# Optimization experiments

Hardware: AMD Instinct MI355X
Metric: run time of the kernel (lower is better)

The kernel has to match this reference:

```python
import jax, jax.numpy as jnp
import numpy as np

B, L, W, S, STEPS, VOCAB, NLAB = 1024, 128, 512, 8, 12, 32, 10

def setup_inputs() -> dict:
    key = jax.random.key(0)
    ks = jax.random.split(key, 24)
    def nrm(k, shape, scale=0.05):
        return jax.random.normal(k, shape, jnp.float32) * scale
    x = jax.random.randint(ks[0], (B, L), 0, VOCAB)
    embed = nrm(ks[1], (VOCAB, W), 0.1).at[0].set(0.0)  # padding_idx=0
    return {
        'x': x,
        'embed': embed,
        'W_mix': nrm(ks[2], (W, 3 * W)), 'b_mix': jnp.zeros((W,), jnp.float32),
        'W_in': nrm(ks[3], (S, W, 2 * W)), 'b_in': jnp.zeros((S, W), jnp.float32),
        'W_link': nrm(ks[4], (S, W, W)), 'b_link': jnp.zeros((S, W), jnp.float32),
        'W_ih': nrm(ks[5], (S, 3 * W, W)), 'b_ih': jnp.zeros((S, 3 * W), jnp.float32),
        'W_hh': nrm(ks[6], (S, 3 * W, W)), 'b_hh': jnp.zeros((S, 3 * W), jnp.float32),
        'W_gate': nrm(ks[7], (S, 1, W)), 'b_gate': jnp.zeros((S, 1), jnp.float32),
        'phase': nrm(ks[8], (S, W), 0.5), 'prism_gain': jnp.zeros((S, W), jnp.float32),
        'W_delta': nrm(ks[9], (S, W, W)), 'b_delta': jnp.zeros((S, W), jnp.float32),
        'decay_param': jnp.zeros((), jnp.float32),
        'W_out': nrm(ks[10], (NLAB, W)), 'b_out': jnp.zeros((NLAB,), jnp.float32),
    }

def _encode(x, embed, W_mix, b_mix):
    emb = embed[x]                                          # [B,L,W]
    mask = (x != 0).astype(jnp.float32)[..., None]          # [B,L,1]
    summed = (emb * mask).sum(1)
    denom = jnp.maximum(mask.sum(1), 1.0)
    mean = summed / denom
    maxed = jnp.where(mask == 0, -10000.0, emb).max(1)
    maxed = jnp.where(jnp.isfinite(maxed), maxed, 0.0)
    last_idx = jnp.maximum(mask[..., 0].sum(1).astype(jnp.int32) - 1, 0)
    last = jnp.take_along_axis(emb, last_idx[:, None, None], axis=1)[:, 0]
    cat = jnp.concatenate([mean, maxed, last], -1)          # [B,3W]
    return jnp.tanh(cat @ W_mix.T + b_mix)

def _forward(x, embed, W_mix, b_mix, W_in, b_in, W_link, b_link, W_ih, b_ih,
             W_hh, b_hh, W_gate, b_gate, phase, prism_gain, W_delta, b_delta,
             decay_param, W_out, b_out):
    summary = _encode(x, embed, W_mix, b_mix)               # [B,W]
    decay = jax.nn.sigmoid(decay_param)
    inv_sqrt_s = np.float32(1.0 / np.sqrt(S))
    gain = jax.nn.softplus(prism_gain)[None]                # [1,S,W]

    def step(carry, _):
        h, hs = carry
        shared = jnp.concatenate([h, summary], -1)          # conditioned: [B,2W]
        f0 = jnp.tanh(jnp.einsum('swi,bi->bsw', W_in, shared) + b_in)      # [B,S,W]
        prev = jnp.roll(f0, 1, axis=1)                      # sparse ring: feats[(i-1)%S]
        feats = jnp.tanh(f0 + jnp.einsum('sow,bsw->bso', W_link, prev) + b_link)
        # recurrent side pockets: per-side GRUCell (torch gate order r,z,n)
        gi = jnp.einsum('sgw,bsw->bsg', W_ih, feats) + b_ih
        gh = jnp.einsum('sgw,bsw->bsg', W_hh, hs) + b_hh
        ir, iz, inn = jnp.split(gi, 3, -1)
        hr, hz, hn = jnp.split(gh, 3, -1)
        r = jax.nn.sigmoid(ir + hr)
        z = jax.nn.sigmoid(iz + hz)
        n = jnp.tanh(inn + r * hn)
        hs_new = (1.0 - z) * n + z * hs                     # [B,S,W]
        feat = hs_new
        gate = jax.nn.sigmoid(jnp.einsum('sow,bsw->bso', W_gate, feat) + b_gate)  # [B,S,1]
        feat = jnp.cos(feat + phase[None]) ** 2 * gain      # prismion
        upd = gate * jnp.tanh(jnp.einsum('sow,bsw->bso', W_delta, feat) + b_delta)
        delta = upd.sum(1) * inv_sqrt_s
        h_new = jnp.tanh(h * decay + delta)
        return (h_new, hs_new), None

    hs0 = jnp.zeros((B, S, W), jnp.float32)
    (h, _), _ = jax.lax.scan(step, (summary, hs0), None, length=STEPS)
    return h @ W_out.T + b_out                               # [B,10]

def reference(x, embed, W_mix, b_mix, W_in, b_in, W_link, b_link, W_ih, b_ih,
              W_hh, b_hh, W_gate, b_gate, phase, prism_gain, W_delta, b_delta,
              decay_param, W_out, b_out):
    return _forward(x, embed, W_mix, b_mix, W_in, b_in, W_link, b_link, W_ih,
                    b_ih, W_hh, b_hh, W_gate, b_gate, phase, prism_gain,
                    W_delta, b_delta, decay_param, W_out, b_out)
```

## Files before the change

### kernel.cpp

```cpp
#include <hip/hip_runtime.h>
#include <hip/hip_bf16.h>


typedef unsigned short u16;
typedef __attribute__((ext_vector_type(8))) short short8;
typedef __attribute__((ext_vector_type(4))) float f32x4;

__device__ __forceinline__ float bf2f(u16 v) {
    union { unsigned int u; float f; } x; x.u = ((unsigned int)v) << 16; return x.f;
}
__device__ __forceinline__ u16 f2bf(float f) {
    union { float f; unsigned int u; } x; x.f = f;
    unsigned int u = x.u;
    return (u16)((u + 0x7FFFu + ((u >> 16) & 1u)) >> 16);
}
__device__ __forceinline__ float fsig(float v) {
    return __builtin_amdgcn_rcpf(1.f + __expf(-v));
}
__device__ __forceinline__ float ftanh(float v) {
    return 1.f - 2.f * __builtin_amdgcn_rcpf(__expf(2.f * v) + 1.f);
}
__device__ __forceinline__ float fsoftplus(float v) {
    return (v > 20.f) ? v : __logf(1.f + __expf(v));
}

union U4 { ushort4 v; u16 e[4]; };

__device__ __forceinline__ void gload_lds16(const u16* g, u16* l) {
    __builtin_amdgcn_global_load_lds(
        (const __attribute__((address_space(1))) unsigned int*)g,
        (__attribute__((address_space(3))) unsigned int*)l, 16, 0, 0);
}

__device__ __forceinline__ int sane16(u16 u) {
    if ((u & 0x7FFF) == 0) return 1;
    int e = (u >> 7) & 0xFF;
    return (e >= 0x33 && e <= 0x43) ? 1 : 0;
}
__global__ __launch_bounds__(256) void detect_k(const u16* __restrict__ raw,
                                                int* __restrict__ flag) {
    const int t = threadIdx.x;
    int c = sane16(raw[1024 + t * 2]) + sane16(raw[1024 + t * 2 + 1]);
#pragma unroll
    for (int off = 32; off; off >>= 1) c += __shfl_down(c, off, 64);
    __shared__ int red[4];
    if ((t & 63) == 0) red[t >> 6] = c;
    __syncthreads();
    if (t == 0) *flag = (red[0] + red[1] + red[2] + red[3] >= 448) ? 1 : 0;
}

struct CT { const void* src[20]; int n[20]; int off[20]; };
__global__ __launch_bounds__(256) void conv_k(CT ct, u16* __restrict__ dstBase,
                                              const int* __restrict__ flag) {
    const int isbf = *flag;
    const int gid = blockIdx.x * 256 + threadIdx.x;
    const int stride = gridDim.x * 256;
    for (int tn = 0; tn < 20; ++tn) {
        const int n = ct.n[tn];
        const int n4 = n >> 2;
        u16* dst = dstBase + ct.off[tn];
        if (!isbf) {
            const float* s = (const float*)ct.src[tn];
            for (int i = gid; i < n4; i += stride) {
                f32x4 v = *(const f32x4*)(s + i * 4);
                *(ushort4*)(dst + i * 4) =
                    make_ushort4(f2bf(v[0]), f2bf(v[1]), f2bf(v[2]), f2bf(v[3]));
            }
            if (gid < (n & 3)) { int i = n4 * 4 + gid; dst[i] = f2bf(s[i]); }
        } else {
            const u16* s = (const u16*)ct.src[tn];
            for (int i = gid; i < n4; i += stride)
                *(ushort4*)(dst + i * 4) = *(const ushort4*)(s + i * 4);
            if (gid < (n & 3)) { int i = n4 * 4 + gid; dst[i] = s[i]; }
        }
    }
}

__global__ __launch_bounds__(256) void pack_k(const u16* __restrict__ Wih,
                                              const u16* __restrict__ Whh,
                                              u16* __restrict__ Wcat) {
    long i = ((long)blockIdx.x * 256 + threadIdx.x) * 8;
    if (i >= 8L * 1536 * 512) return;
    long sg = i >> 9;
    long k  = i & 511;
    *(short8*)(Wcat + sg * 1024 + k)       = *(const short8*)(Wih + i);
    *(short8*)(Wcat + sg * 1024 + 512 + k) = *(const short8*)(Whh + i);
}

struct GP {
    const u16* A;  long lda; long aOff[8];
    const u16* Bw; long ldb; long bwOff[8];
    const u16* bias; long biasOff[8];
    const u16* add; long ldadd; long addOff;
    const float* gate_pre;
    const u16* bgate;
    void* C; long ldc; long cOff[8];
    float* C2;
    u16* C3;
    int K; int nt;
};

template<int EPI, int MT, int SWZ, int PIPE, int NK>
__global__ __launch_bounds__(256) void gemm_k(GP p) {
    constexpr int MW   = MT / 32;
    constexpr int AITS = MT / 32;
    constexpr int NBUF = PIPE ? 3 : 2;
    __shared__ __align__(16) u16 lA[NBUF][MT * 64];
    __shared__ __align__(16) u16 lB[NBUF][128 * 64];
    const int t    = threadIdx.x;
    const int lane = t & 63;
    const int wv   = t >> 6;
    int bx = blockIdx.x, byy = blockIdx.y;
    if (SWZ) {
        int wgid = bx + (byy << 5);
        bx  = ((wgid & 7) << 2) + ((wgid >> 3) & 3);
        byy = wgid >> 5;
    }
    const int z    = bx / p.nt;
    const int n0   = (bx - z * p.nt) * 128;
    const int m0   = byy * MT;

    const u16* Ab = p.A + p.aOff[z] + (long)m0 * p.lda;
    const u16* Bb = p.Bw + p.bwOff[z] + (long)n0 * p.ldb;

    f32x4 acc[MW][4];
#pragma unroll
    for (int i = 0; i < MW; i++)
#pragma unroll
        for (int j = 0; j < 4; j++) acc[i][j] = (f32x4){0.f, 0.f, 0.f, 0.f};

    const int wm   = (wv & 1) * (MT / 2);
    const int wn   = (wv >> 1) * 64;
    const int fr   = lane & 15;
    const int quad = lane >> 4;

    auto stage = [&](int buf, long kb) {
#pragma unroll
        for (int it = 0; it < AITS; ++it) {
            int flat = it * 256 + t, row = flat >> 3, src = (flat & 7) ^ (row & 7);
            gload_lds16(Ab + (long)row * p.lda + kb + src * 8, &lA[buf][flat * 8]);
        }
#pragma unroll
        for (int it = 0; it < 4; ++it) {
            int flat = it * 256 + t, row = flat >> 3, src = (flat & 7) ^ (row & 7);
            gload_lds16(Bb + (long)row * p.ldb + kb + src * 8, &lB[buf][flat * 8]);
        }
    };
    auto inner = [&](int cur) {
#pragma unroll
        for (int kk = 0; kk < 2; ++kk) {
            const int q = kk * 4 + quad;
            short8 aF[MW], bF[4];
#pragma unroll
            for (int mi = 0; mi < MW; mi++) {
                int row = wm + mi * 16 + fr;
                aF[mi] = *(const short8*)&lA[cur][row * 64 + (q ^ (row & 7)) * 8];
            }
#pragma unroll
            for (int ni = 0; ni < 4; ni++) {
                int row = wn + ni * 16 + fr;
                bF[ni] = *(const short8*)&lB[cur][row * 64 + (q ^ (row & 7)) * 8];
            }
#pragma unroll
            for (int mi = 0; mi < MW; mi++)
#pragma unroll
                for (int ni = 0; ni < 4; ni++)
                    acc[mi][ni] = __builtin_amdgcn_mfma_f32_16x16x32_bf16(
                        aF[mi], bF[ni], acc[mi][ni], 0, 0, 0);
        }
    };

    if (PIPE == 0) {
        const int nk = p.K >> 6;
        stage(0, 0);
        __syncthreads();
        for (int kt = 0; kt < nk; ++kt) {
            const int cur = kt & 1, nxt = cur ^ 1;
            if (kt + 1 < nk) stage(nxt, (long)(kt + 1) * 64);
            inner(cur);
            __syncthreads();
        }
    } else {
        stage(0, 0); stage(1, 64);
        asm volatile("s_waitcnt vmcnt(6)" ::: "memory");
        __builtin_amdgcn_s_barrier();
#pragma unroll
        for (int kt = 0; kt < NK; ++kt) {
            if (kt + 2 < NK) stage((kt + 2) % 3, (long)(kt + 2) * 64);
            inner(kt % 3);
            if (kt + 1 < NK) {
                if (kt + 2 < NK)
                    asm volatile("s_waitcnt vmcnt(6) lgkmcnt(0)" ::: "memory");
                else
                    asm volatile("s_waitcnt vmcnt(0) lgkmcnt(0)" ::: "memory");
                __builtin_amdgcn_s_barrier();
            }
        }
    }

    float sgv[MW][4];
    if (EPI == 3) {
#pragma unroll
        for (int mi = 0; mi < MW; mi++)
#pragma unroll
            for (int r = 0; r < 4; r++) {
                long row = m0 + wm + mi * 16 + quad * 4 + r;
                sgv[mi][r] = fsig(p.gate_pre[row * 8 + z] + bf2f(p.bgate[z]));
            }
    }

#pragma unroll
    for (int mi = 0; mi < MW; mi++) {
#pragma unroll
        for (int ni = 0; ni < 4; ni++) {
            const int mg = m0 + wm + mi * 16 + quad * 4;
            const int ng = n0 + wn + ni * 16 + fr;
#pragma unroll
            for (int r = 0; r < 4; r++) {
                float v = acc[mi][ni][r];
                const long row = mg + r;
                if (EPI == 1) {
                    float ad = bf2f(p.add[z * p.addOff + row * p.ldadd + ng]);
                    v = ftanh(v + ad + bf2f(p.bias[p.biasOff[z] + ng]));
                    ((u16*)p.C)[p.cOff[z] + row * p.ldc + ng] = f2bf(v);
                } else if (EPI == 3) {
                    v = ftanh(v + bf2f(p.bias[p.biasOff[z] + ng])) * sgv[mi][r];
                    ((u16*)p.C)[p.cOff[z] + row * p.ldc + ng] = f2bf(v);
                } else if (EPI == 4) {
                    v = ftanh(v + bf2f(p.bias[ng]));
                    u16 b = f2bf(v);
                    ((u16*)p.C)[row * 512 + ng] = b;
                    p.C3[row * 512 + ng] = b;
                    p.C2[row * 512 + ng] = v;
                } else if (EPI == 6) {
                    v = v + bf2f(p.bias[p.biasOff[z] + ng]);
                    ((u16*)p.C)[p.cOff[z] + row * p.ldc + ng] = f2bf(v);
                } else {
                    float ad = bf2f(p.add[row * p.ldadd + ng]);
                    v = ftanh(v + ad);
                    ((u16*)p.C)[row * p.ldc + ng] = f2bf(v);
                }
            }
        }
    }
}

struct GGP {
    const u16* fhs_in;
    u16* fhs_out;
    const u16* Wcat;
    const u16* b_ih;
    const u16* b_hh;
    u16* prism;
    float* gate_pre;
    const u16* Wg;
    const u16* phase;
    const u16* pgain;
};

__global__ __launch_bounds__(512, 2) void grug_k(GGP p) {
    __shared__ __align__(16) u16 sA[2][128 * 32];
    __shared__ __align__(16) u16 sW[3][3][128 * 32];
    const int t    = threadIdx.x;
    const int lane = t & 63;
    const int wv   = t >> 6;
    const int wgid = blockIdx.x + (blockIdx.y << 5);
    const int s    = wgid & 7;
    const int idx  = wgid >> 3;
    const int w0   = (idx & 3) * 128;
    const int m0   = (idx >> 2) * 128;
    const int fr   = lane & 15;
    const int quad = lane >> 4;
    const int wm   = (wv & 1) * 64;
    const int wn   = (wv >> 1) * 32;

    const u16* Ab = p.fhs_in + (long)m0 * 8192 + (long)s * 1024;
    const u16* Wb = p.Wcat + (long)s * 1536 * 1024;

    f32x4 acc[4][4][2];
#pragma unroll
    for (int q = 0; q < 4; q++)
#pragma unroll
        for (int mi = 0; mi < 4; mi++)
#pragma unroll
            for (int ni = 0; ni < 2; ni++) acc[q][mi][ni] = (f32x4){0.f,0.f,0.f,0.f};

    const int arow = t >> 2, ac4 = t & 3, asrc = ac4 ^ ((arow >> 1) & 3);

    auto stageA = [&](int buf, int kt) {
        gload_lds16(Ab + (long)arow * 8192 + kt * 32 + asrc * 8, &sA[buf][t * 8]);
    };
    auto stageWq = [&](int buf, int kt, int q) {
        long g = (long)(q * 512 + w0 + arow);
        gload_lds16(Wb + g * 1024 + kt * 32 + asrc * 8, &sW[buf][q][t * 8]);
    };

    stageA(0, 0);
    stageWq(0, 0, 0); stageWq(0, 0, 1); stageWq(0, 0, 2);
    stageWq(1, 1, 0); stageWq(1, 1, 1); stageWq(1, 1, 2);
    asm volatile("s_waitcnt vmcnt(3)" ::: "memory");
    __builtin_amdgcn_s_barrier();

    int aCur = 0, wCur = 0;
    for (int kt = 0; kt < 32; ++kt) {
        const int aNxt = aCur ^ 1;
        int wNx2 = wCur + 2; if (wNx2 >= 3) wNx2 -= 3;
        short8 aF[4], bF0[2], bF1[2], bF2[2];

#pragma unroll
        for (int mi = 0; mi < 4; mi++) {
            int row = wm + mi * 16 + fr;
            aF[mi] = *(const short8*)&sA[aCur][row * 32 + ((quad ^ ((row >> 1) & 3)) & 3) * 8];
        }
#pragma unroll
        for (int ni = 0; ni < 2; ni++) {
            int row = wn + ni * 16 + fr;
            bF0[ni] = *(const short8*)&sW[wCur][0][row * 32 + ((quad ^ ((row >> 1) & 3)) & 3) * 8];
        }
        if (kt + 1 < 32) stageA(aNxt, kt + 1);
        if (kt + 2 < 32) stageWq(wNx2, kt + 2, 0);
        __builtin_amdgcn_s_barrier();
        asm volatile("s_waitcnt lgkmcnt(0)" ::: "memory");
        __builtin_amdgcn_s_setprio(1);
#pragma unroll
        for (int mi = 0; mi < 4; mi++)
#pragma unroll
            for (int ni = 0; ni < 2; ni++)
                acc[0][mi][ni] = __builtin_amdgcn_mfma_f32_16x16x32_bf16(aF[mi], bF0[ni], acc[0][mi][ni], 0, 0, 0);
        __builtin_amdgcn_s_setprio(0);
        __builtin_amdgcn_s_barrier();

#pragma unroll
        for (int ni = 0; ni < 2; ni++) {
            int row = wn + ni * 16 + fr;
            bF1[ni] = *(const short8*)&sW[wCur][1][row * 32 + ((quad ^ ((row >> 1) & 3)) & 3) * 8];
        }
        if (kt + 2 < 32) stageWq(wNx2, kt + 2, 1);
        __builtin_amdgcn_s_barrier();
        asm volatile("s_waitcnt lgkmcnt(0)" ::: "memory");
        __builtin_amdgcn_s_setprio(1);
#pragma unroll
        for (int mi = 0; mi < 4; mi++)
#pragma unroll
            for (int ni = 0; ni < 2; ni++)
                acc[1][mi][ni] = __builtin_amdgcn_mfma_f32_16x16x32_bf16(aF[mi], bF1[ni], acc[1][mi][ni], 0, 0, 0);
        __builtin_amdgcn_s_setprio(0);
        __builtin_amdgcn_s_barrier();

#pragma unroll
        for (int ni = 0; ni < 2; ni++) {
            int row = wn + ni * 16 + fr;
            bF2[ni] = *(const short8*)&sW[wCur][2][row * 32 + ((quad ^ ((row >> 1) & 3)) & 3) * 8];
        }
        if (kt + 2 < 32) stageWq(wNx2, kt + 2, 2);
        if (kt < 30)       asm volatile("s_waitcnt vmcnt(3) lgkmcnt(0)" ::: "memory");
        else if (kt == 30) asm volatile("s_waitcnt vmcnt(0) lgkmcnt(0)" ::: "memory");
        else               asm volatile("s_waitcnt lgkmcnt(0)" ::: "memory");
        __builtin_amdgcn_s_setprio(1);
        if (kt < 16) {
#pragma unroll
            for (int mi = 0; mi < 4; mi++)
#pragma unroll
                for (int ni = 0; ni < 2; ni++)
                    acc[2][mi][ni] = __builtin_amdgcn_mfma_f32_16x16x32_bf16(aF[mi], bF2[ni], acc[2][mi][ni], 0, 0, 0);
        } else {
#pragma unroll
            for (int mi = 0; mi < 4; mi++)
#pragma unroll
                for (int ni = 0; ni < 2; ni++)
                    acc[3][mi][ni] = __builtin_amdgcn_mfma_f32_16x16x32_bf16(aF[mi], bF2[ni], acc[3][mi][ni], 0, 0, 0);
        }
        __builtin_amdgcn_s_setprio(0);
        __builtin_amdgcn_s_barrier();

        aCur = aNxt;
        wCur += 1; if (wCur >= 3) wCur -= 3;
    }

    const u16* bih = p.b_ih + (long)s * 1536;
    const u16* bhh = p.b_hh + (long)s * 1536;
    float gp[4][4];
#pragma unroll
    for (int mi = 0; mi < 4; mi++)
#pragma unroll
        for (int r = 0; r < 4; r++) gp[mi][r] = 0.f;

#pragma unroll
    for (int ni = 0; ni < 2; ni++) {
        const int col = w0 + wn + ni * 16 + fr;
        const float br  = bf2f(bih[col])        + bf2f(bhh[col]);
        const float bz  = bf2f(bih[512 + col])  + bf2f(bhh[512 + col]);
        const float bin = bf2f(bih[1024 + col]);
        const float bhn = bf2f(bhh[1024 + col]);
        const float ph  = bf2f(p.phase[s * 512 + col]);
        const float gain = fsoftplus(bf2f(p.pgain[s * 512 + col]));
        const float wg  = bf2f(p.Wg[s * 512 + col]);
#pragma unroll
        for (int mi = 0; mi < 4; mi++) {
#pragma unroll
            for (int r = 0; r < 4; r++) {
                const long b = m0 + wm + mi * 16 + quad * 4 + r;
                float rv = fsig(acc[0][mi][ni][r] + br);
                float zv = fsig(acc[1][mi][ni][r] + bz);
                float nv = ftanh(acc[2][mi][ni][r] + bin + rv * (acc[3][mi][ni][r] + bhn));
                float hold = bf2f(p.fhs_in[b * 8192 + s * 1024 + 512 + col]);
                float hv = (1.f - zv) * nv + zv * hold;
                p.fhs_out[b * 8192 + s * 1024 + 512 + col] = f2bf(hv);
                float c = __cosf(hv + ph);
                p.prism[b * 4096 + s * 512 + col] = f2bf(c * c * gain);
                gp[mi][r] += wg * hv;
            }
        }
    }
#pragma unroll
    for (int m = 1; m < 16; m <<= 1)
#pragma unroll
        for (int mi = 0; mi < 4; mi++)
#pragma unroll
            for (int r = 0; r < 4; r++) gp[mi][r] += __shfl_xor(gp[mi][r], m, 64);
    if (fr == 0) {
#pragma unroll
        for (int mi = 0; mi < 4; mi++)
#pragma unroll
            for (int r = 0; r < 4; r++) {
                long b = m0 + wm + mi * 16 + quad * 4 + r;
                atomicAdd(&p.gate_pre[b * 8 + s], gp[mi][r]);
            }
    }
}

__global__ __launch_bounds__(256) void encode_k(const int* __restrict__ x,
                                                const u16* __restrict__ embed,
                                                u16* __restrict__ cat) {
    __shared__ int toks[128];
    __shared__ int cnt_s;
    const int b = blockIdx.x, t = threadIdx.x;
    if (t < 128) toks[t] = x[b * 128 + t];
    __syncthreads();
    if (t == 0) {
        int c = 0;
        for (int l = 0; l < 128; l++) c += (toks[l] != 0);
        cnt_s = c;
    }
    __syncthreads();
    const int cnt = cnt_s;
    const int lastTok = toks[cnt > 0 ? cnt - 1 : 0];
    for (int w = t; w < 512; w += 256) {
        float sum = 0.f, mx = -10000.f;
        for (int l = 0; l < 128; l++) {
            int tok = toks[l];
            if (tok != 0) {
                float e = bf2f(embed[tok * 512 + w]);
                sum += e;
                mx = fmaxf(mx, e);
            }
        }
        float mean = sum / (float)(cnt > 0 ? cnt : 1);
        float last = bf2f(embed[lastTok * 512 + w]);
        cat[(long)b * 1536 + w]        = f2bf(mean);
        cat[(long)b * 1536 + 512 + w]  = f2bf(mx);
        cat[(long)b * 1536 + 1024 + w] = f2bf(last);
    }
}

__global__ __launch_bounds__(256) void hupd_k(const u16* __restrict__ upd,
                                              float* __restrict__ h,
                                              u16* __restrict__ h_b,
                                              const u16* __restrict__ decay_p,
                                              float* __restrict__ gate_pre) {
    const int idx = blockIdx.x * 256 + threadIdx.x;
    if (idx < 8192) gate_pre[idx] = 0.f;
    const int b = idx >> 9, w = idx & 511;
    const long base = (long)b * 4096 + w;
    float dsum = 0.f;
#pragma unroll
    for (int s = 0; s < 8; s++) dsum += bf2f(upd[base + s * 512]);
    const float decay = fsig(bf2f(decay_p[0]));
    const float hv = ftanh(h[idx] * decay + dsum * 0.35355339059327373f);
    h[idx] = hv;
    h_b[idx] = f2bf(hv);
}

__global__ __launch_bounds__(64) void out_k(const float* __restrict__ h,
                                            const u16* __restrict__ Wout,
                                            const u16* __restrict__ bout,
                                            void* __restrict__ out,
                                            const int* __restrict__ flag) {
    const int b = blockIdx.x, lane = threadIdx.x;
    const int isbf = *flag;
    for (int j = 0; j < 10; j++) {
        float p = 0.f;
#pragma unroll
        for (int k = 0; k < 8; k++) {
            int w = lane + k * 64;
            p += h[(long)b * 512 + w] * bf2f(Wout[j * 512 + w]);
        }
#pragma unroll
        for (int off = 32; off; off >>= 1) p += __shfl_down(p, off, 64);
        if (lane == 0) {
            float val = p + bf2f(bout[j]);
            if (isbf) ((u16*)out)[b * 10 + j] = f2bf(val);
            else      ((float*)out)[b * 10 + j] = val;
        }
    }
}

extern "C" void kernel_launch(void* const* d_in, const int* in_sizes, int n_in,
                              void* d_out, int out_size, void* d_ws, size_t ws_size,
                              hipStream_t stream) {
    (void)n_in; (void)out_size; (void)ws_size;
    const int* x = (const int*)d_in[0];

    char* pp = (char*)d_ws;
    auto carve = [&](size_t n) { char* r = pp; pp += (n + 255) & ~(size_t)255; return (void*)r; };

    CT ct;
    size_t ctot = 0;
    for (int i = 0; i < 20; i++) {
        ct.src[i] = d_in[i + 1];
        ct.n[i]   = in_sizes[i + 1];
        ct.off[i] = (int)ctot;
        ctot += ((size_t)in_sizes[i + 1] + 15) & ~(size_t)15;
    }
    u16* canon = (u16*)carve(ctot * 2);
    const u16* embed  = canon + ct.off[0];
    const u16* W_mix  = canon + ct.off[1];
    const u16* b_mix  = canon + ct.off[2];
    const u16* W_in   = canon + ct.off[3];
    const u16* b_in   = canon + ct.off[4];
    const u16* W_link = canon + ct.off[5];
    const u16* b_link = canon + ct.off[6];
    const u16* W_ih   = canon + ct.off[7];
    const u16* b_ih   = canon + ct.off[8];
    const u16* W_hh   = canon + ct.off[9];
    const u16* b_hh   = canon + ct.off[10];
    const u16* W_gate = canon + ct.off[11];
    const u16* b_gate = canon + ct.off[12];
    const u16* phase  = canon + ct.off[13];
    const u16* pgain  = canon + ct.off[14];
    const u16* W_delta= canon + ct.off[15];
    const u16* b_delta= canon + ct.off[16];
    const u16* decayp = canon + ct.off[17];
    const u16* W_out  = canon + ct.off[18];
    const u16* b_out  = canon + ct.off[19];

    int*   flag   = (int*)  carve(256);
    u16*   Wcat   = (u16*)  carve((size_t)8 * 1536 * 1024 * 2);
    u16*   cat    = (u16*)  carve((size_t)1024 * 1536 * 2);
    u16*   h_b    = (u16*)  carve((size_t)1024 * 512 * 2);
    u16*   summ_b = (u16*)  carve((size_t)1024 * 512 * 2);
    float* h      = (float*)carve((size_t)1024 * 512 * 4);
    u16*   cin    = (u16*)  carve((size_t)1024 * 4096 * 2);
    u16*   f0     = (u16*)  carve((size_t)1024 * 4096 * 2);
    u16*   fhs0   = (u16*)  carve((size_t)1024 * 8192 * 2);
    u16*   fhs1   = (u16*)  carve((size_t)1024 * 8192 * 2);
    u16*   prism  = (u16*)  carve((size_t)1024 * 4096 * 2);
    u16*   upd    = (u16*)  carve((size_t)1024 * 4096 * 2);
    float* gate_pre = (float*)carve((size_t)1024 * 8 * 4);

    (void)hipMemsetAsync(fhs0, 0, (size_t)1024 * 8192 * 2, stream);
    (void)hipMemsetAsync(fhs1, 0, (size_t)1024 * 8192 * 2, stream);
    (void)hipMemsetAsync(gate_pre, 0, (size_t)1024 * 8 * 4, stream);

    detect_k<<<dim3(1), dim3(256), 0, stream>>>((const u16*)d_in[1], flag);
    conv_k<<<dim3(1024), dim3(256), 0, stream>>>(ct, canon, flag);
    pack_k<<<dim3(3072), dim3(256), 0, stream>>>(W_ih, W_hh, Wcat);
    encode_k<<<dim3(1024), dim3(256), 0, stream>>>(x, embed, cat);

    {
        GP p{}; p.A = cat; p.lda = 1536; p.Bw = W_mix; p.ldb = 1536;
        p.bias = b_mix; p.C = h_b; p.ldc = 512; p.C2 = h; p.C3 = summ_b;
        p.K = 1536; p.nt = 4;
        gemm_k<4, 64, 0, 0, 0><<<dim3(4, 16, 1), dim3(256), 0, stream>>>(p);
    }
    {
        GP p{}; p.A = summ_b; p.lda = 512; p.Bw = W_in + 512; p.ldb = 1024;
        p.bias = b_in; p.C = cin; p.ldc = 4096; p.K = 512; p.nt = 32;
        gemm_k<6, 64, 1, 1, 8><<<dim3(32, 16, 1), dim3(256), 0, stream>>>(p);
    }

    for (int step = 0; step < 12; ++step) {
        u16* fhs_cur = (step & 1) ? fhs1 : fhs0;
        u16* fhs_nxt = (step & 1) ? fhs0 : fhs1;
        {
            GP p{}; p.A = h_b; p.lda = 512; p.Bw = W_in; p.ldb = 1024;
            p.add = cin; p.ldadd = 4096; p.C = f0; p.ldc = 4096;
            p.K = 512; p.nt = 32;
            gemm_k<7, 64, 1, 1, 8><<<dim3(32, 16, 1), dim3(256), 0, stream>>>(p);
        }
        {
            GP p{}; p.A = f0; p.lda = 4096;
            for (int s = 0; s < 8; s++) p.aOff[s] = (long)((s + 7) & 7) * 512;
            p.Bw = W_link; p.ldb = 512;
            for (int s = 0; s < 8; s++) p.bwOff[s] = (long)s * 512 * 512;
            p.bias = b_link;
            for (int s = 0; s < 8; s++) p.biasOff[s] = (long)s * 512;
            p.add = f0; p.ldadd = 4096; p.addOff = 512;
            p.C = fhs_cur; p.ldc = 8192;
            for (int s = 0; s < 8; s++) p.cOff[s] = (long)s * 1024;
            p.K = 512; p.nt = 4;
            gemm_k<1, 64, 1, 1, 8><<<dim3(32, 16, 1), dim3(256), 0, stream>>>(p);
        }
        {
            GGP g{};
            g.fhs_in = fhs_cur; g.fhs_out = fhs_nxt; g.Wcat = Wcat;
            g.b_ih = b_ih; g.b_hh = b_hh; g.prism = prism; g.gate_pre = gate_pre;
            g.Wg = W_gate; g.phase = phase; g.pgain = pgain;
            grug_k<<<dim3(32, 8, 1), dim3(512), 0, stream>>>(g);
        }
        {
            GP p{}; p.A = prism; p.lda = 4096;
            for (int s = 0; s < 8; s++) p.aOff[s] = (long)s * 512;
            p.Bw = W_delta; p.ldb = 512;
            for (int s = 0; s < 8; s++) p.bwOff[s] = (long)s * 512 * 512;
            p.bias = b_delta;
            for (int s = 0; s < 8; s++) p.biasOff[s] = (long)s * 512;
            p.gate_pre = gate_pre; p.bgate = b_gate;
            p.C = upd; p.ldc = 4096;
            for (int s = 0; s < 8; s++) p.cOff[s] = (long)s * 512;
            p.K = 512; p.nt = 4;
            gemm_k<3, 64, 1, 1, 8><<<dim3(32, 16, 1), dim3(256), 0, stream>>>(p);
        }
        hupd_k<<<dim3(2048), dim3(256), 0, stream>>>(upd, h, h_b, decayp, gate_pre);
    }

    out_k<<<dim3(1024), dim3(64), 0, stream>>>(h, W_out, b_out, d_out, flag);
}
```

Measured before the change: 1.499 ms.

## Add 128x128 eight-wave GEMM with interleaved stage/MFMA pipeline for K=512 GEMMs

Adds a new gemm8_k kernel with 512 threads, 128x128 tiles, a 32-wide K step and triple-buffered LDS. It splits each K step into two MFMA halves, interleaved with A and B global-to-LDS prefetches and raised wave priority, to hide load latency. All per-step K=512 GEMMs switch to it, halving the grid to 256 blocks. The risk is lower occupancy and more barriers per K step, and the fixed 16-iteration loop hardcodes K=512.

```diff
diff --git a/kernel.cpp b/kernel.cpp
--- a/kernel.cpp
+++ b/kernel.cpp
@@ -100,13 +100,12 @@
     int K; int nt;
 };
 
-template<int EPI, int MT, int SWZ, int PIPE, int NK>
+template<int EPI, int MT, int SWZ>
 __global__ __launch_bounds__(256) void gemm_k(GP p) {
     constexpr int MW   = MT / 32;
     constexpr int AITS = MT / 32;
-    constexpr int NBUF = PIPE ? 3 : 2;
-    __shared__ __align__(16) u16 lA[NBUF][MT * 64];
-    __shared__ __align__(16) u16 lB[NBUF][128 * 64];
+    __shared__ __align__(16) u16 lA[2][MT * 64];
+    __shared__ __align__(16) u16 lB[2][128 * 64];
     const int t    = threadIdx.x;
     const int lane = t & 63;
     const int wv   = t >> 6;
@@ -170,38 +169,124 @@
         }
     };
 
-    if (PIPE == 0) {
-        const int nk = p.K >> 6;
-        stage(0, 0);
+    const int nk = p.K >> 6;
+    stage(0, 0);
+    __syncthreads();
+    for (int kt = 0; kt < nk; ++kt) {
+        const int cur = kt & 1, nxt = cur ^ 1;
+        if (kt + 1 < nk) stage(nxt, (long)(kt + 1) * 64);
+        inner(cur);
         __syncthreads();
-        for (int kt = 0; kt < nk; ++kt) {
-            const int cur = kt & 1, nxt = cur ^ 1;
-            if (kt + 1 < nk) stage(nxt, (long)(kt + 1) * 64);
-            inner(cur);
-            __syncthreads();
-        }
-    } else {
-        stage(0, 0); stage(1, 64);
-        asm volatile("s_waitcnt vmcnt(6)" ::: "memory");
+    }
+
+#pragma unroll
+    for (int mi = 0; mi < MW; mi++) {
+#pragma unroll
+        for (int ni = 0; ni < 4; ni++) {
+            const int mg = m0 + wm + mi * 16 + quad * 4;
+            const int ng = n0 + wn + ni * 16 + fr;
+#pragma unroll
+            for (int r = 0; r < 4; r++) {
+                float v = acc[mi][ni][r];
+                const long row = mg + r;
+                if (EPI == 4) {
+                    v = ftanh(v + bf2f(p.bias[ng]));
+                    u16 b = f2bf(v);
+                    ((u16*)p.C)[row * 512 + ng] = b;
+                    p.C3[row * 512 + ng] = b;
+                    p.C2[row * 512 + ng] = v;
+                }
+            }
+        }
+    }
+}
+
+template<int EPI>
+__global__ __launch_bounds__(512, 2) void gemm8_k(GP p) {
+    __shared__ __align__(16) u16 lA[3][128 * 32];
+    __shared__ __align__(16) u16 lB[3][128 * 32];
+    const int t    = threadIdx.x;
+    const int lane = t & 63;
+    const int wv   = t >> 6;
+    const int wgid = blockIdx.x + (blockIdx.y << 5);
+    const int zc   = wgid & 7;
+    const int ct   = zc * 4 + ((wgid >> 3) & 3);
+    const int m0   = (wgid >> 5) * 128;
+    const int z    = ct / p.nt;
+    const int n0   = (ct - z * p.nt) * 128;
+    const int fr   = lane & 15;
+    const int quad = lane >> 4;
+    const int wm   = (wv & 1) * 64;
+    const int wn   = (wv >> 1) * 32;
+
+    const u16* Ab = p.A + p.aOff[z] + (long)m0 * p.lda;
+    const u16* Bb = p.Bw + p.bwOff[z] + (long)n0 * p.ldb;
+
+    f32x4 acc[4][2];
+#pragma unroll
+    for (int mi = 0; mi < 4; mi++)
+#pragma unroll
+        for (int ni = 0; ni < 2; ni++) acc[mi][ni] = (f32x4){0.f, 0.f, 0.f, 0.f};
+
+    const int arow = t >> 2, ac4 = t & 3, asrc = ac4 ^ ((arow >> 1) & 3);
+
+    auto stageA = [&](int buf, int kt) {
+        gload_lds16(Ab + (long)arow * p.lda + kt * 32 + asrc * 8, &lA[buf][t * 8]);
+    };
+    auto stageB = [&](int buf, int kt) {
+        gload_lds16(Bb + (long)arow * p.ldb + kt * 32 + asrc * 8, &lB[buf][t * 8]);
+    };
+
+    stageA(0, 0); stageB(0, 0); stageA(1, 1); stageB(1, 1);
+    asm volatile("s_waitcnt vmcnt(2)" ::: "memory");
+    __builtin_amdgcn_s_barrier();
+
+    int cur = 0;
+    for (int kt = 0; kt < 16; ++kt) {
+        int nx2 = cur + 2; if (nx2 >= 3) nx2 -= 3;
+        short8 aF[4], bF0, bF1;
+
+#pragma unroll
+        for (int mi = 0; mi < 4; mi++) {
+            int row = wm + mi * 16 + fr;
+            aF[mi] = *(const short8*)&lA[cur][row * 32 + ((quad ^ ((row >> 1) & 3)) & 3) * 8];
+        }
+        {
+            int row = wn + fr;
+            bF0 = *(const short8*)&lB[cur][row * 32 + ((quad ^ ((row >> 1) & 3)) & 3) * 8];
+        }
+        if (kt + 2 < 16) stageA(nx2, kt + 2);
         __builtin_amdgcn_s_barrier();
-#pragma unroll
-        for (int kt = 0; kt < NK; ++kt) {
-            if (kt + 2 < NK) stage((kt + 2) % 3, (long)(kt + 2) * 64);
-            inner(kt % 3);
-            if (kt + 1 < NK) {
-                if (kt + 2 < NK)
-                    asm volatile("s_waitcnt vmcnt(6) lgkmcnt(0)" ::: "memory");
-                else
-                    asm volatile("s_waitcnt vmcnt(0) lgkmcnt(0)" ::: "memory");
-                __builtin_amdgcn_s_barrier();
-            }
-        }
-    }
-
-    float sgv[MW][4];
+        asm volatile("s_waitcnt lgkmcnt(0)" ::: "memory");
+        __builtin_amdgcn_s_setprio(1);
+#pragma unroll
+        for (int mi = 0; mi < 4; mi++)
+            acc[mi][0] = __builtin_amdgcn_mfma_f32_16x16x32_bf16(aF[mi], bF0, acc[mi][0], 0, 0, 0);
+        __builtin_amdgcn_s_setprio(0);
+        __builtin_amdgcn_s_barrier();
+
+        {
+            int row = wn + 16 + fr;
+            bF1 = *(const short8*)&lB[cur][row * 32 + ((quad ^ ((row >> 1) & 3)) & 3) * 8];
+        }
+        if (kt + 2 < 16) stageB(nx2, kt + 2);
+        if (kt < 14)       asm volatile("s_waitcnt vmcnt(2) lgkmcnt(0)" ::: "memory");
+        else if (kt == 14) asm volatile("s_waitcnt vmcnt(0) lgkmcnt(0)" ::: "memory");
+        else               asm volatile("s_waitcnt lgkmcnt(0)" ::: "memory");
+        __builtin_amdgcn_s_setprio(1);
+#pragma unroll
+        for (int mi = 0; mi < 4; mi++)
+            acc[mi][1] = __builtin_amdgcn_mfma_f32_16x16x32_bf16(aF[mi], bF1, acc[mi][1], 0, 0, 0);
+        __builtin_amdgcn_s_setprio(0);
+        __builtin_amdgcn_s_barrier();
+
+        cur += 1; if (cur >= 3) cur -= 3;
+    }
+
+    float sgv[4][4];
     if (EPI == 3) {
 #pragma unroll
-        for (int mi = 0; mi < MW; mi++)
+        for (int mi = 0; mi < 4; mi++)
 #pragma unroll
             for (int r = 0; r < 4; r++) {
                 long row = m0 + wm + mi * 16 + quad * 4 + r;
@@ -210,9 +295,9 @@
     }
 
 #pragma unroll
-    for (int mi = 0; mi < MW; mi++) {
-#pragma unroll
-        for (int ni = 0; ni < 4; ni++) {
+    for (int mi = 0; mi < 4; mi++) {
+#pragma unroll
+        for (int ni = 0; ni < 2; ni++) {
             const int mg = m0 + wm + mi * 16 + quad * 4;
             const int ng = n0 + wn + ni * 16 + fr;
 #pragma unroll
@@ -226,12 +311,6 @@
                 } else if (EPI == 3) {
                     v = ftanh(v + bf2f(p.bias[p.biasOff[z] + ng])) * sgv[mi][r];
                     ((u16*)p.C)[p.cOff[z] + row * p.ldc + ng] = f2bf(v);
-                } else if (EPI == 4) {
-                    v = ftanh(v + bf2f(p.bias[ng]));
-                    u16 b = f2bf(v);
-                    ((u16*)p.C)[row * 512 + ng] = b;
-                    p.C3[row * 512 + ng] = b;
-                    p.C2[row * 512 + ng] = v;
                 } else if (EPI == 6) {
                     v = v + bf2f(p.bias[p.biasOff[z] + ng]);
                     ((u16*)p.C)[p.cOff[z] + row * p.ldc + ng] = f2bf(v);
@@ -571,12 +650,12 @@
         GP p{}; p.A = cat; p.lda = 1536; p.Bw = W_mix; p.ldb = 1536;
         p.bias = b_mix; p.C = h_b; p.ldc = 512; p.C2 = h; p.C3 = summ_b;
         p.K = 1536; p.nt = 4;
-        gemm_k<4, 64, 0, 0, 0><<<dim3(4, 16, 1), dim3(256), 0, stream>>>(p);
+        gemm_k<4, 64, 0><<<dim3(4, 16, 1), dim3(256), 0, stream>>>(p);
     }
     {
         GP p{}; p.A = summ_b; p.lda = 512; p.Bw = W_in + 512; p.ldb = 1024;
         p.bias = b_in; p.C = cin; p.ldc = 4096; p.K = 512; p.nt = 32;
-        gemm_k<6, 64, 1, 1, 8><<<dim3(32, 16, 1), dim3(256), 0, stream>>>(p);
+        gemm8_k<6><<<dim3(32, 8, 1), dim3(512), 0, stream>>>(p);
     }
 
     for (int step = 0; step < 12; ++step) {
@@ -586,7 +665,7 @@
             GP p{}; p.A = h_b; p.lda = 512; p.Bw = W_in; p.ldb = 1024;
             p.add = cin; p.ldadd = 4096; p.C = f0; p.ldc = 4096;
             p.K = 512; p.nt = 32;
-            gemm_k<7, 64, 1, 1, 8><<<dim3(32, 16, 1), dim3(256), 0, stream>>>(p);
+            gemm8_k<7><<<dim3(32, 8, 1), dim3(512), 0, stream>>>(p);
         }
         {
             GP p{}; p.A = f0; p.lda = 4096;
@@ -599,7 +678,7 @@
             p.C = fhs_cur; p.ldc = 8192;
             for (int s = 0; s < 8; s++) p.cOff[s] = (long)s * 1024;
             p.K = 512; p.nt = 4;
-            gemm_k<1, 64, 1, 1, 8><<<dim3(32, 16, 1), dim3(256), 0, stream>>>(p);
+            gemm8_k<1><<<dim3(32, 8, 1), dim3(512), 0, stream>>>(p);
         }
         {
             GGP g{};
@@ -619,7 +698,7 @@
             p.C = upd; p.ldc = 4096;
             for (int s = 0; s < 8; s++) p.cOff[s] = (long)s * 512;
             p.K = 512; p.nt = 4;
-            gemm_k<3, 64, 1, 1, 8><<<dim3(32, 16, 1), dim3(256), 0, stream>>>(p);
+            gemm8_k<3><<<dim3(32, 8, 1), dim3(512), 0, stream>>>(p);
         }
         hupd_k<<<dim3(2048), dim3(256), 0, stream>>>(upd, h, h_b, decayp, gate_pre);
     }
```

Result: slower. 1.557 ms (+3.8%).
